# Kernel tuning notes

Measured on AMD Instinct MI355X. Metric: run time of the kernel, lower is better.

The kernel has to match this reference:

```python
import jax, jax.numpy as jnp
import numpy as np

B, N, NODE_DIM, EDGE_DIM, HID = 32, 100, 128, 64, 128
EPS = 1e-5


def _bn(x, gamma, beta):
    # training-mode BatchNorm1d over all leading dims (biased variance)
    d = x.shape[-1]
    xf = x.reshape(-1, d)
    mean = xf.mean(axis=0)
    var = ((xf - mean) ** 2).mean(axis=0)
    return ((x - mean) * jax.lax.rsqrt(var + EPS)) * gamma + beta


def setup_inputs() -> dict:
    key = jax.random.key(0)
    ks = jax.random.split(key, 12)
    s = lambda fan_in: 1.0 / np.sqrt(fan_in)
    return {
        "h": jax.random.normal(ks[0], (B, N, NODE_DIM), jnp.float32),
        "e": jax.random.normal(ks[1], (B, N, N, EDGE_DIM), jnp.float32),
        "adj": (jax.random.uniform(ks[2], (B, N, N)) < 0.3).astype(jnp.float32),
        "WU": jax.random.uniform(ks[3], (HID, NODE_DIM), jnp.float32, -s(NODE_DIM), s(NODE_DIM)),
        "WV": jax.random.uniform(ks[4], (HID, NODE_DIM), jnp.float32, -s(NODE_DIM), s(NODE_DIM)),
        "WA": jax.random.uniform(ks[5], (HID, NODE_DIM), jnp.float32, -s(NODE_DIM), s(NODE_DIM)),
        "WB": jax.random.uniform(ks[6], (HID, NODE_DIM), jnp.float32, -s(NODE_DIM), s(NODE_DIM)),
        "WC": jax.random.uniform(ks[7], (HID, EDGE_DIM), jnp.float32, -s(EDGE_DIM), s(EDGE_DIM)),
        "bn_edge_gamma": jnp.ones((HID,), jnp.float32),
        "bn_edge_beta": jnp.zeros((HID,), jnp.float32),
        "bn_node_gamma": jnp.ones((HID,), jnp.float32),
        "bn_node_beta": jnp.zeros((HID,), jnp.float32),
    }


def reference(h, e, adj, WU, WV, WA, WB, WC,
              bn_edge_gamma, bn_edge_beta, bn_node_gamma, bn_node_beta):
    # e_new[b,m,n,d] = C(e) + A(h_m) + B(h_n)
    eh = (jnp.einsum('bmne,de->bmnd', e, WC)
          + jnp.einsum('bmc,dc->bmd', h, WA)[:, :, None, :]
          + jnp.einsum('bnc,dc->bnd', h, WB)[:, None, :, :])
    eh = jax.nn.relu(_bn(eh, bn_edge_gamma, bn_edge_beta))
    eh = eh * adj[..., None]
    e_weight = jax.nn.sigmoid(eh)
    e_norm = jax.nn.softmax(e_weight, axis=2)  # softmax over neighbor dim n
    h_in = jnp.einsum('bmc,dc->bmd', h, WU)
    h_nb = jnp.einsum('bnc,dc->bnd', h, WV)
    m = jnp.einsum('bmnd,bnd->bmd', e_norm, h_nb)
    m = _bn(m, bn_node_gamma, bn_node_beta)
    h_out = h_in + jax.nn.relu(m)
    return (h_out, e_norm)
```

## Files before the change

kernel.cpp:

```cpp
#include <hip/hip_runtime.h>
#include <math.h>

#define B_   32
#define N_   100
#define ND_  128
#define ED_  64
#define HID_ 128
#define EPS_ 1e-5f
#define NNODE (B_*N_)
#define EDGE_SAMPLES ((float)(B_*N_*N_))
#define LOG2E_ 1.4426950408889634f

#define WS_A      0
#define WS_PK     409600
#define WS_HIN    819200
#define WS_M      1638400
#define WS_STATS  2048000
#define WS_SCSH   (WS_STATS + 8192)
#define WS_NSTB   (WS_SCSH + 256)
#define ZERO_CNT  (8192 + 256 + 8192)

typedef __attribute__((ext_vector_type(8))) short bf16x8;
typedef __attribute__((ext_vector_type(4))) float f32x4;
#define MFMA16(a,b,c) __builtin_amdgcn_mfma_f32_16x16x32_bf16(a,b,c,0,0,0)

__device__ __forceinline__ unsigned short f2bf(float f) {
  unsigned int u = __float_as_uint(f);
  unsigned int r = (u + 0x7fffu + ((u >> 16) & 1u)) >> 16;
  return (unsigned short)r;
}

__device__ __forceinline__ void load_wc_frags(const float* __restrict__ WC,
                                              int d0, int lg, bf16x8 bfr[2]) {
#pragma unroll
  for (int kb = 0; kb < 2; ++kb) {
    const float* wrow = WC + d0 * 64 + kb * 32 + lg * 8;
    float4 u0 = *(const float4*)wrow;
    float4 u1 = *(const float4*)(wrow + 4);
    bf16x8 f;
    f[0] = (short)f2bf(u0.x); f[1] = (short)f2bf(u0.y);
    f[2] = (short)f2bf(u0.z); f[3] = (short)f2bf(u0.w);
    f[4] = (short)f2bf(u1.x); f[5] = (short)f2bf(u1.y);
    f[6] = (short)f2bf(u1.z); f[7] = (short)f2bf(u1.w);
    bfr[kb] = f;
  }
}

__device__ __forceinline__ void stage_row512(const float4 ld[4],
                                             unsigned short* dst, int t) {
#pragma unroll
  for (int k = 0; k < 4; ++k) {
    int i = t + k * 512;
    if (i < 1600) {
      float4 v = ld[k];
      int row = i >> 4, col = (i & 15) * 4;
      *(ushort4*)&dst[row * 72 + col] =
          make_ushort4(f2bf(v.x), f2bf(v.y), f2bf(v.z), f2bf(v.w));
    }
  }
}

__device__ __forceinline__ void mfma_row(const unsigned short* src,
                                         const bf16x8 bfr[2], f32x4 acc[7],
                                         int lr, int lg) {
#pragma unroll
  for (int mt = 0; mt < 7; ++mt) {
    int row = mt * 16 + lr;
    bf16x8 af0 = *(const bf16x8*)&src[row * 72 + lg * 8];
    bf16x8 af1 = *(const bf16x8*)&src[row * 72 + 32 + lg * 8];
    f32x4 a = (f32x4)0.f;
    a = MFMA16(af0, bfr[0], a);
    a = MFMA16(af1, bfr[1], a);
    acc[mt] = a;
  }
}

__global__ __launch_bounds__(256) void k1_proj(
    const float* __restrict__ h,
    const float* __restrict__ WA, const float* __restrict__ WB,
    const float* __restrict__ WU, const float* __restrict__ WV,
    float* __restrict__ ws) {
  __shared__ unsigned short h_lds[64 * 136];
  __shared__ unsigned short w_lds[128 * 136];
  const int t  = threadIdx.x;
  const int r0 = blockIdx.x * 64;
  const int y  = blockIdx.y;
  const float* W = (y == 0) ? WA : (y == 1) ? WB : (y == 2) ? WU : WV;

  {
    int gid = (y * 50 + blockIdx.x) * 256 + t;
    if (gid < ZERO_CNT) ws[WS_STATS + gid] = 0.f;
  }

  const float4* hp = (const float4*)(h + (size_t)r0 * 128);
  const float4* wp = (const float4*)W;
#pragma unroll
  for (int k = 0; k < 8; ++k) {
    int i = t + k * 256;
    int row = i >> 5, col = (i & 31) * 4;
    float4 v = hp[i];
    *(ushort4*)&h_lds[row * 136 + col] =
        make_ushort4(f2bf(v.x), f2bf(v.y), f2bf(v.z), f2bf(v.w));
  }
#pragma unroll
  for (int k = 0; k < 16; ++k) {
    int i = t + k * 256;
    int row = i >> 5, col = (i & 31) * 4;
    float4 u = wp[i];
    *(ushort4*)&w_lds[row * 136 + col] =
        make_ushort4(f2bf(u.x), f2bf(u.y), f2bf(u.z), f2bf(u.w));
  }
  __syncthreads();

  const int w  = t >> 6;
  const int l  = t & 63;
  const int lr = l & 15;
  const int lg = l >> 4;

  bf16x8 bfr[2][4];
#pragma unroll
  for (int nt = 0; nt < 2; ++nt) {
    int d = w * 32 + nt * 16 + lr;
#pragma unroll
    for (int kb = 0; kb < 4; ++kb)
      bfr[nt][kb] = *(const bf16x8*)&w_lds[d * 136 + kb * 32 + lg * 8];
  }

  f32x4 acc[4][2];
#pragma unroll
  for (int mt = 0; mt < 4; ++mt) { acc[mt][0] = (f32x4)0.f; acc[mt][1] = (f32x4)0.f; }

#pragma unroll
  for (int mt = 0; mt < 4; ++mt) {
    int row = mt * 16 + lr;
    bf16x8 af[4];
#pragma unroll
    for (int kb = 0; kb < 4; ++kb)
      af[kb] = *(const bf16x8*)&h_lds[row * 136 + kb * 32 + lg * 8];
#pragma unroll
    for (int nt = 0; nt < 2; ++nt)
#pragma unroll
      for (int kb = 0; kb < 4; ++kb)
        acc[mt][nt] = MFMA16(af[kb], bfr[nt][kb], acc[mt][nt]);
  }

  if (y == 0 || y == 2) {
    float* outp = ws + ((y == 0) ? WS_A : WS_HIN);
#pragma unroll
    for (int mt = 0; mt < 4; ++mt)
#pragma unroll
      for (int nt = 0; nt < 2; ++nt) {
        int dcol = w * 32 + nt * 16 + lr;
#pragma unroll
        for (int j = 0; j < 4; ++j) {
          int row = r0 + mt * 16 + lg * 4 + j;
          outp[row * 128 + dcol] = acc[mt][nt][j];
        }
      }
  } else {
    unsigned short* pks = (unsigned short*)(ws + WS_PK);
    const int half = (y == 1) ? 0 : 1;
#pragma unroll
    for (int mt = 0; mt < 4; ++mt)
#pragma unroll
      for (int nt = 0; nt < 2; ++nt) {
        int dcol = w * 32 + nt * 16 + lr;
#pragma unroll
        for (int j = 0; j < 4; ++j) {
          int row = r0 + mt * 16 + lg * 4 + j;
          pks[(row * 128 + dcol) * 2 + half] = f2bf(acc[mt][nt][j]);
        }
      }
  }
}

__global__ __launch_bounds__(512) void k2_stats(
    const float* __restrict__ e, const float* __restrict__ WC,
    float* __restrict__ ws) {
  __shared__ unsigned short e_lds[2][112 * 72];
  const int t   = threadIdx.x;
  const int b   = blockIdx.x;
  const int bm0 = b * N_ + blockIdx.y * 2;
  const int w   = t >> 6;
  const int l   = t & 63;
  const int lr  = l & 15;
  const int lg  = l >> 4;
  const int d0  = w * 16 + lr;

  float4 ld[4];
  const float4* e0 = (const float4*)(e + (size_t)bm0 * (N_ * ED_));
#pragma unroll
  for (int k = 0; k < 4; ++k) { int i = t + k * 512; if (i < 1600) ld[k] = e0[i]; }

  unsigned int pk[7][4];
  const unsigned int* pkp = (const unsigned int*)(ws + WS_PK) + b * (N_ * 128);
#pragma unroll
  for (int mt = 0; mt < 7; ++mt)
#pragma unroll
    for (int j = 0; j < 4; ++j) {
      int node = mt * 16 + lg * 4 + j;
      pk[mt][j] = (node < N_) ? pkp[node * 128 + d0] : 0u;
    }
  const float Aa = ws[WS_A + bm0 * 128 + d0];
  const float Ab = ws[WS_A + (bm0 + 1) * 128 + d0];

  bf16x8 bfr[2];
  load_wc_frags(WC, d0, lg, bfr);

  for (int i = t; i < 12 * 72; i += 512) {
    e_lds[0][100 * 72 + i] = 0;
    e_lds[1][100 * 72 + i] = 0;
  }

  stage_row512(ld, e_lds[0], t);
  const float4* e1 = (const float4*)(e + (size_t)(bm0 + 1) * (N_ * ED_));
#pragma unroll
  for (int k = 0; k < 4; ++k) { int i = t + k * 512; if (i < 1600) ld[k] = e1[i]; }
  __syncthreads();

  f32x4 acc[7];
  float s = 0.f, ssq = 0.f;

  mfma_row(e_lds[0], bfr, acc, lr, lg);
  stage_row512(ld, e_lds[1], t);
#pragma unroll
  for (int mt = 0; mt < 7; ++mt)
#pragma unroll
    for (int j = 0; j < 4; ++j) {
      int node = mt * 16 + lg * 4 + j;
      if (node < N_) {
        float x = acc[mt][j] + Aa + __uint_as_float(pk[mt][j] << 16);
        s += x; ssq += x * x;
      }
    }
  __syncthreads();

  mfma_row(e_lds[1], bfr, acc, lr, lg);
#pragma unroll
  for (int mt = 0; mt < 7; ++mt)
#pragma unroll
    for (int j = 0; j < 4; ++j) {
      int node = mt * 16 + lg * 4 + j;
      if (node < N_) {
        float x = acc[mt][j] + Ab + __uint_as_float(pk[mt][j] << 16);
        s += x; ssq += x * x;
      }
    }

  s   += __shfl_xor(s, 16);   s   += __shfl_xor(s, 32);
  ssq += __shfl_xor(ssq, 16); ssq += __shfl_xor(ssq, 32);
  if (l < 16) {
    atomicAdd(&ws[WS_STATS + b * 256 + d0], s);
    atomicAdd(&ws[WS_STATS + b * 256 + 128 + d0], ssq);
  }
}

__global__ __launch_bounds__(128) void k0_finalize(
    const float* __restrict__ gamma_e, const float* __restrict__ beta_e,
    float* __restrict__ ws) {
  const int t = threadIdx.x;
  float S = 0.f, SS = 0.f;
#pragma unroll
  for (int j = 0; j < 32; ++j) {
    S  += ws[WS_STATS + j * 256 + t];
    SS += ws[WS_STATS + j * 256 + 128 + t];
  }
  float mean = S * (1.0f / EDGE_SAMPLES);
  float var  = SS * (1.0f / EDGE_SAMPLES) - mean * mean;
  float sc   = gamma_e[t] * rsqrtf(var + EPS_);
  ws[WS_SCSH + t]       = sc;
  ws[WS_SCSH + 128 + t] = beta_e[t] - mean * sc;
}

__global__ __launch_bounds__(512) void k4_main(
    const float* __restrict__ e, const float* __restrict__ adj,
    const float* __restrict__ WC,
    float* __restrict__ ws, float* __restrict__ out_enorm) {
  __shared__ unsigned short e_lds[112 * 72];
  __shared__ float adj_lds[112];
  const int t  = threadIdx.x;
  const int bm = (blockIdx.x & 7) * 400 + (blockIdx.x >> 3);
  const int b  = bm / N_;
  const int w  = t >> 6;
  const int l  = t & 63;
  const int lr = l & 15;
  const int lg = l >> 4;
  const int d0 = w * 16 + lr;

  float4 ld[4];
  const float4* ef4 = (const float4*)(e + (size_t)bm * (N_ * ED_));
#pragma unroll
  for (int k = 0; k < 4; ++k) { int i = t + k * 512; if (i < 1600) ld[k] = ef4[i]; }

  unsigned int pk[7][4];
  const unsigned int* pkp = (const unsigned int*)(ws + WS_PK) + b * (N_ * 128);
#pragma unroll
  for (int mt = 0; mt < 7; ++mt)
#pragma unroll
    for (int j = 0; j < 4; ++j) {
      int node = mt * 16 + lg * 4 + j;
      pk[mt][j] = (node < N_) ? pkp[node * 128 + d0] : 0u;
    }
  const float A0  = ws[WS_A + bm * 128 + d0];
  const float sc0 = ws[WS_SCSH + d0];
  const float sh0 = ws[WS_SCSH + 128 + d0];

  bf16x8 bfr[2];
  load_wc_frags(WC, d0, lg, bfr);

  if (t < 112) adj_lds[t] = (t < N_) ? adj[bm * N_ + t] : 0.f;

  stage_row512(ld, e_lds, t);
  for (int i = t; i < 12 * 72; i += 512) e_lds[100 * 72 + i] = 0;
  __syncthreads();

  f32x4 acc[7];
  mfma_row(e_lds, bfr, acc, lr, lg);

  float den = 0.f;
#pragma unroll
  for (int mt = 0; mt < 7; ++mt)
#pragma unroll
    for (int j = 0; j < 4; ++j) {
      int node = mt * 16 + lg * 4 + j;
      float bv = __uint_as_float(pk[mt][j] << 16);
      float x  = (acc[mt][j] + A0 + bv) * sc0 + sh0;
      float r  = fmaxf(x, 0.f) * adj_lds[node];
      float en = __builtin_amdgcn_exp2f(r * -LOG2E_);
      float sg = __builtin_amdgcn_rcpf(1.f + en);
      float p  = __builtin_amdgcn_exp2f(sg * LOG2E_);
      acc[mt][j] = p; den += p;
    }
  den += __shfl_xor(den, 16); den += __shfl_xor(den, 32);
  den -= 12.f * __builtin_amdgcn_exp2f(0.5f * LOG2E_);
  const float rc = __builtin_amdgcn_rcpf(den);

  float msg = 0.f;
  float* outp = out_enorm + (size_t)bm * (N_ * 128);
#pragma unroll
  for (int mt = 0; mt < 7; ++mt)
#pragma unroll
    for (int j = 0; j < 4; ++j) {
      int node = mt * 16 + lg * 4 + j;
      if (node < N_) {
        float v = acc[mt][j] * rc;
        outp[node * 128 + d0] = v;
        float hn = __uint_as_float(pk[mt][j] & 0xffff0000u);
        msg += v * hn;
      }
    }
  msg += __shfl_xor(msg, 16); msg += __shfl_xor(msg, 32);
  if (l < 16) {
    ws[WS_M + bm * 128 + d0] = msg;
    atomicAdd(&ws[WS_NSTB + b * 256 + d0],       msg);
    atomicAdd(&ws[WS_NSTB + b * 256 + 128 + d0], msg * msg);
  }
}

__global__ __launch_bounds__(256) void k5b_hout(
    const float* __restrict__ gamma_n, const float* __restrict__ beta_n,
    const float* __restrict__ ws, float* __restrict__ hout) {
  __shared__ float sc_l[128], sh_l[128];
  const int t = threadIdx.x;
  if (t < 128) {
    float S = 0.f, SS = 0.f;
#pragma unroll
    for (int j = 0; j < 32; ++j) {
      S  += ws[WS_NSTB + j * 256 + t];
      SS += ws[WS_NSTB + j * 256 + 128 + t];
    }
    float mean = S * (1.0f / (float)NNODE);
    float var  = SS * (1.0f / (float)NNODE) - mean * mean;
    float sc   = gamma_n[t] * rsqrtf(var + EPS_);
    sc_l[t] = sc;
    sh_l[t] = beta_n[t] - mean * sc;
  }
  __syncthreads();
  const int idx = blockIdx.x * 256 + t;
  const int d = t & 127;
  float mv = ws[WS_M + idx];
  hout[idx] = ws[WS_HIN + idx] + fmaxf(mv * sc_l[d] + sh_l[d], 0.f);
}

extern "C" void kernel_launch(void* const* d_in, const int* in_sizes, int n_in,
                              void* d_out, int out_size, void* d_ws, size_t ws_size,
                              hipStream_t stream) {
  (void)in_sizes; (void)n_in; (void)out_size; (void)ws_size;
  const float* h   = (const float*)d_in[0];
  const float* e   = (const float*)d_in[1];
  const float* adj = (const float*)d_in[2];
  const float* WU  = (const float*)d_in[3];
  const float* WV  = (const float*)d_in[4];
  const float* WA  = (const float*)d_in[5];
  const float* WB  = (const float*)d_in[6];
  const float* WC  = (const float*)d_in[7];
  const float* geg = (const float*)d_in[8];
  const float* geb = (const float*)d_in[9];
  const float* gng = (const float*)d_in[10];
  const float* gnb = (const float*)d_in[11];

  float* out = (float*)d_out;
  float* ws  = (float*)d_ws;

  k1_proj    <<<dim3(50, 4),  256, 0, stream>>>(h, WA, WB, WU, WV, ws);
  k2_stats   <<<dim3(32, 50), 512, 0, stream>>>(e, WC, ws);
  k0_finalize<<<1,            128, 0, stream>>>(geg, geb, ws);
  k4_main    <<<3200,         512, 0, stream>>>(e, adj, WC, ws, out + 409600);
  k5b_hout   <<<1600,         256, 0, stream>>>(gng, gnb, ws, out);
}
```

Measured before the change: 97.21 us.

## Fuse BN finalize into stats kernel, coarsen stats and projection blocks

Measured after the change: 169.4 us. +74.2%, slower.

```diff
diff --git a/kernel.cpp b/kernel.cpp
--- a/kernel.cpp
+++ b/kernel.cpp
@@ -11,6 +11,9 @@
 #define EDGE_SAMPLES ((float)(B_*N_*N_))
 #define LOG2E_ 1.4426950408889634f
 
+#define MC_   7
+#define K2_BLOCKS (32*15)
+
 #define WS_A      0
 #define WS_PK     409600
 #define WS_HIN    819200
@@ -18,7 +21,8 @@
 #define WS_STATS  2048000
 #define WS_SCSH   (WS_STATS + 8192)
 #define WS_NSTB   (WS_SCSH + 256)
-#define ZERO_CNT  (8192 + 256 + 8192)
+#define WS_CNT    (WS_NSTB + 8192)
+#define ZERO_CNT  (8192 + 256 + 8192 + 64)
 
 typedef __attribute__((ext_vector_type(8))) short bf16x8;
 typedef __attribute__((ext_vector_type(4))) float f32x4;
@@ -80,32 +84,27 @@
     const float* __restrict__ WA, const float* __restrict__ WB,
     const float* __restrict__ WU, const float* __restrict__ WV,
     float* __restrict__ ws) {
-  __shared__ unsigned short h_lds[64 * 136];
+  __shared__ unsigned short h_lds[128 * 136];
   __shared__ unsigned short w_lds[128 * 136];
   const int t  = threadIdx.x;
-  const int r0 = blockIdx.x * 64;
+  const int r0 = blockIdx.x * 128;
   const int y  = blockIdx.y;
   const float* W = (y == 0) ? WA : (y == 1) ? WB : (y == 2) ? WU : WV;
 
   {
-    int gid = (y * 50 + blockIdx.x) * 256 + t;
+    int gid = (y * 25 + blockIdx.x) * 256 + t;
     if (gid < ZERO_CNT) ws[WS_STATS + gid] = 0.f;
   }
 
   const float4* hp = (const float4*)(h + (size_t)r0 * 128);
   const float4* wp = (const float4*)W;
 #pragma unroll
-  for (int k = 0; k < 8; ++k) {
+  for (int k = 0; k < 16; ++k) {
     int i = t + k * 256;
     int row = i >> 5, col = (i & 31) * 4;
     float4 v = hp[i];
     *(ushort4*)&h_lds[row * 136 + col] =
         make_ushort4(f2bf(v.x), f2bf(v.y), f2bf(v.z), f2bf(v.w));
-  }
-#pragma unroll
-  for (int k = 0; k < 16; ++k) {
-    int i = t + k * 256;
-    int row = i >> 5, col = (i & 31) * 4;
     float4 u = wp[i];
     *(ushort4*)&w_lds[row * 136 + col] =
         make_ushort4(f2bf(u.x), f2bf(u.y), f2bf(u.z), f2bf(u.w));
@@ -126,12 +125,12 @@
       bfr[nt][kb] = *(const bf16x8*)&w_lds[d * 136 + kb * 32 + lg * 8];
   }
 
-  f32x4 acc[4][2];
-#pragma unroll
-  for (int mt = 0; mt < 4; ++mt) { acc[mt][0] = (f32x4)0.f; acc[mt][1] = (f32x4)0.f; }
-
-#pragma unroll
-  for (int mt = 0; mt < 4; ++mt) {
+  f32x4 acc[8][2];
+#pragma unroll
+  for (int mt = 0; mt < 8; ++mt) { acc[mt][0] = (f32x4)0.f; acc[mt][1] = (f32x4)0.f; }
+
+#pragma unroll
+  for (int mt = 0; mt < 8; ++mt) {
     int row = mt * 16 + lr;
     bf16x8 af[4];
 #pragma unroll
@@ -147,7 +146,7 @@
   if (y == 0 || y == 2) {
     float* outp = ws + ((y == 0) ? WS_A : WS_HIN);
 #pragma unroll
-    for (int mt = 0; mt < 4; ++mt)
+    for (int mt = 0; mt < 8; ++mt)
 #pragma unroll
       for (int nt = 0; nt < 2; ++nt) {
         int dcol = w * 32 + nt * 16 + lr;
@@ -161,7 +160,7 @@
     unsigned short* pks = (unsigned short*)(ws + WS_PK);
     const int half = (y == 1) ? 0 : 1;
 #pragma unroll
-    for (int mt = 0; mt < 4; ++mt)
+    for (int mt = 0; mt < 8; ++mt)
 #pragma unroll
       for (int nt = 0; nt < 2; ++nt) {
         int dcol = w * 32 + nt * 16 + lr;
@@ -176,21 +175,27 @@
 
 __global__ __launch_bounds__(512) void k2_stats(
     const float* __restrict__ e, const float* __restrict__ WC,
+    const float* __restrict__ gamma_e, const float* __restrict__ beta_e,
     float* __restrict__ ws) {
   __shared__ unsigned short e_lds[2][112 * 72];
-  const int t   = threadIdx.x;
-  const int b   = blockIdx.x;
-  const int bm0 = b * N_ + blockIdx.y * 2;
-  const int w   = t >> 6;
-  const int l   = t & 63;
-  const int lr  = l & 15;
-  const int lg  = l >> 4;
-  const int d0  = w * 16 + lr;
+  __shared__ int last_s;
+  const int t    = threadIdx.x;
+  const int b    = blockIdx.x;
+  const int m0   = blockIdx.y * MC_;
+  const int mcnt = min(MC_, N_ - m0);
+  const int bm0  = b * N_ + m0;
+  const int w    = t >> 6;
+  const int l    = t & 63;
+  const int lr   = l & 15;
+  const int lg   = l >> 4;
+  const int d0   = w * 16 + lr;
 
   float4 ld[4];
-  const float4* e0 = (const float4*)(e + (size_t)bm0 * (N_ * ED_));
-#pragma unroll
-  for (int k = 0; k < 4; ++k) { int i = t + k * 512; if (i < 1600) ld[k] = e0[i]; }
+  {
+    const float4* e0 = (const float4*)(e + (size_t)bm0 * (N_ * ED_));
+#pragma unroll
+    for (int k = 0; k < 4; ++k) { int i = t + k * 512; if (i < 1600) ld[k] = e0[i]; }
+  }
 
   unsigned int pk[7][4];
   const unsigned int* pkp = (const unsigned int*)(ws + WS_PK) + b * (N_ * 128);
@@ -201,8 +206,10 @@
       int node = mt * 16 + lg * 4 + j;
       pk[mt][j] = (node < N_) ? pkp[node * 128 + d0] : 0u;
     }
-  const float Aa = ws[WS_A + bm0 * 128 + d0];
-  const float Ab = ws[WS_A + (bm0 + 1) * 128 + d0];
+  float Ar[MC_];
+#pragma unroll
+  for (int r = 0; r < MC_; ++r)
+    Ar[r] = (r < mcnt) ? ws[WS_A + (bm0 + r) * 128 + d0] : 0.f;
 
   bf16x8 bfr[2];
   load_wc_frags(WC, d0, lg, bfr);
@@ -212,40 +219,32 @@
     e_lds[1][100 * 72 + i] = 0;
   }
 
-  stage_row512(ld, e_lds[0], t);
-  const float4* e1 = (const float4*)(e + (size_t)(bm0 + 1) * (N_ * ED_));
-#pragma unroll
-  for (int k = 0; k < 4; ++k) { int i = t + k * 512; if (i < 1600) ld[k] = e1[i]; }
-  __syncthreads();
-
-  f32x4 acc[7];
   float s = 0.f, ssq = 0.f;
-
-  mfma_row(e_lds[0], bfr, acc, lr, lg);
-  stage_row512(ld, e_lds[1], t);
-#pragma unroll
-  for (int mt = 0; mt < 7; ++mt)
-#pragma unroll
-    for (int j = 0; j < 4; ++j) {
-      int node = mt * 16 + lg * 4 + j;
-      if (node < N_) {
-        float x = acc[mt][j] + Aa + __uint_as_float(pk[mt][j] << 16);
-        s += x; ssq += x * x;
+  int buf = 0;
+  for (int r = 0; r < mcnt; ++r) {
+    stage_row512(ld, e_lds[buf], t);
+    __syncthreads();
+    if (r + 1 < mcnt) {
+      const float4* nxt = (const float4*)(e + (size_t)(bm0 + r + 1) * (N_ * ED_));
+#pragma unroll
+      for (int k = 0; k < 4; ++k) { int i = t + k * 512; if (i < 1600) ld[k] = nxt[i]; }
+    }
+
+    f32x4 acc[7];
+    mfma_row(e_lds[buf], bfr, acc, lr, lg);
+    const float A0 = Ar[r];
+#pragma unroll
+    for (int mt = 0; mt < 7; ++mt)
+#pragma unroll
+      for (int j = 0; j < 4; ++j) {
+        int node = mt * 16 + lg * 4 + j;
+        if (node < N_) {
+          float x = acc[mt][j] + A0 + __uint_as_float(pk[mt][j] << 16);
+          s += x; ssq += x * x;
+        }
       }
-    }
-  __syncthreads();
-
-  mfma_row(e_lds[1], bfr, acc, lr, lg);
-#pragma unroll
-  for (int mt = 0; mt < 7; ++mt)
-#pragma unroll
-    for (int j = 0; j < 4; ++j) {
-      int node = mt * 16 + lg * 4 + j;
-      if (node < N_) {
-        float x = acc[mt][j] + Ab + __uint_as_float(pk[mt][j] << 16);
-        s += x; ssq += x * x;
-      }
-    }
+    buf ^= 1;
+  }
 
   s   += __shfl_xor(s, 16);   s   += __shfl_xor(s, 32);
   ssq += __shfl_xor(ssq, 16); ssq += __shfl_xor(ssq, 32);
@@ -253,23 +252,27 @@
     atomicAdd(&ws[WS_STATS + b * 256 + d0], s);
     atomicAdd(&ws[WS_STATS + b * 256 + 128 + d0], ssq);
   }
-}
-
-__global__ __launch_bounds__(128) void k0_finalize(
-    const float* __restrict__ gamma_e, const float* __restrict__ beta_e,
-    float* __restrict__ ws) {
-  const int t = threadIdx.x;
-  float S = 0.f, SS = 0.f;
-#pragma unroll
-  for (int j = 0; j < 32; ++j) {
-    S  += ws[WS_STATS + j * 256 + t];
-    SS += ws[WS_STATS + j * 256 + 128 + t];
-  }
-  float mean = S * (1.0f / EDGE_SAMPLES);
-  float var  = SS * (1.0f / EDGE_SAMPLES) - mean * mean;
-  float sc   = gamma_e[t] * rsqrtf(var + EPS_);
-  ws[WS_SCSH + t]       = sc;
-  ws[WS_SCSH + 128 + t] = beta_e[t] - mean * sc;
+
+  __syncthreads();
+  __threadfence();
+  if (t == 0) {
+    unsigned int tk = atomicAdd((unsigned int*)&ws[WS_CNT], 1u);
+    last_s = (tk == K2_BLOCKS - 1);
+  }
+  __syncthreads();
+  if (last_s && t < 128) {
+    float S = 0.f, SS = 0.f;
+#pragma unroll
+    for (int j = 0; j < 32; ++j) {
+      S  += ws[WS_STATS + j * 256 + t];
+      SS += ws[WS_STATS + j * 256 + 128 + t];
+    }
+    float mean = S * (1.0f / EDGE_SAMPLES);
+    float var  = SS * (1.0f / EDGE_SAMPLES) - mean * mean;
+    float sc   = gamma_e[t] * rsqrtf(var + EPS_);
+    ws[WS_SCSH + t]       = sc;
+    ws[WS_SCSH + 128 + t] = beta_e[t] - mean * sc;
+  }
 }
 
 __global__ __launch_bounds__(512) void k4_main(
@@ -279,7 +282,7 @@
   __shared__ unsigned short e_lds[112 * 72];
   __shared__ float adj_lds[112];
   const int t  = threadIdx.x;
-  const int bm = (blockIdx.x & 7) * 400 + (blockIdx.x >> 3);
+  const int bm = blockIdx.x;
   const int b  = bm / N_;
   const int w  = t >> 6;
   const int l  = t & 63;
@@ -402,9 +405,8 @@
   float* out = (float*)d_out;
   float* ws  = (float*)d_ws;
 
-  k1_proj    <<<dim3(50, 4),  256, 0, stream>>>(h, WA, WB, WU, WV, ws);
-  k2_stats   <<<dim3(32, 50), 512, 0, stream>>>(e, WC, ws);
-  k0_finalize<<<1,            128, 0, stream>>>(geg, geb, ws);
-  k4_main    <<<3200,         512, 0, stream>>>(e, adj, WC, ws, out + 409600);
-  k5b_hout   <<<1600,         256, 0, stream>>>(gng, gnb, ws, out);
-}
+  k1_proj <<<dim3(25, 4),  256, 0, stream>>>(h, WA, WB, WU, WV, ws);
+  k2_stats<<<dim3(32, 15), 512, 0, stream>>>(e, WC, geg, geb, ws);
+  k4_main <<<3200,         512, 0, stream>>>(e, adj, WC, ws, out + 409600);
+  k5b_hout<<<1600,         256, 0, stream>>>(gng, gnb, ws, out);
+}
```
